# Performance work log

Measured on AMD Instinct MI355X. Metric: run time of the kernel, lower is better.

## Reference

```python
import jax, jax.numpy as jnp
import numpy as np

LN_EPS = 1e-5
ATT_EPS = 1e-6

def layer_norm(x, scale, bias):
    mu = jnp.mean(x, axis=-1, keepdims=True)
    var = jnp.mean(jnp.square(x - mu), axis=-1, keepdims=True)
    return (x - mu) * jax.lax.rsqrt(var + LN_EPS) * scale + bias

def setup_inputs() -> dict:
    key = jax.random.key(0)
    ks = jax.random.split(key, 8)
    N, C, H = 16384, 1024, 8
    s = 0.02
    return {
        "x": jax.random.normal(ks[0], (N, C), dtype=jnp.float32),
        "Wq": jax.random.normal(ks[1], (C, C), dtype=jnp.float32) * s,
        "Wkv": jax.random.normal(ks[2], (C, 2 * C), dtype=jnp.float32) * s,
        "ln1_scale": jnp.ones((C,), dtype=jnp.float32),
        "ln1_bias": jnp.zeros((C,), dtype=jnp.float32),
        "W1": jax.random.normal(ks[3], (C, C), dtype=jnp.float32) * s,
        "b1": jnp.zeros((C,), dtype=jnp.float32),
        "W2": jax.random.normal(ks[4], (C, C), dtype=jnp.float32) * s,
        "b2": jnp.zeros((C,), dtype=jnp.float32),
        "ln2_scale": jnp.ones((C,), dtype=jnp.float32),
        "ln2_bias": jnp.zeros((C,), dtype=jnp.float32),
    }

def reference(x, Wq, Wkv, ln1_scale, ln1_bias, W1, b1, W2, b2, ln2_scale, ln2_bias):
    H = 8
    N, C = x.shape
    d = C // H
    # QKV projections; torch .view(-1, d, heads) splits last dim as (d, H)
    q = (x @ Wq).reshape(N, d, H)
    kv = x @ Wkv  # [N, 2C]
    k = kv[:, :C].reshape(N, d, H)
    v = kv[:, C:].reshape(N, d, H)
    # Kernelized linear attention per head (phi = elu + 1), global segment (bi=None)
    phi_q = jax.nn.elu(q) + 1.0
    phi_k = jax.nn.elu(k) + 1.0
    kv_sum = jnp.einsum('ndh,neh->deh', phi_k, v)      # [d, d, H]
    z = jnp.sum(phi_k, axis=0)                          # [d, H]
    num = jnp.einsum('ndh,deh->neh', phi_q, kv_sum)     # [N, d, H]
    den = jnp.einsum('ndh,dh->nh', phi_q, z)            # [N, H]
    t = (num / (den[:, None, :] + ATT_EPS)).reshape(N, C)
    # AddNorm (beta=False, dropout=0): ln(t + x)
    y = layer_norm(t + x, ln1_scale, ln1_bias)
    # FFN: Linear -> GELU (exact) -> Linear
    h = jax.nn.gelu(y @ W1 + b1, approximate=False)
    f = h @ W2 + b2
    return layer_norm(f + y, ln2_scale, ln2_bias)
```

## Files before the change

kernel.cpp:

```cpp
#include <hip/hip_runtime.h>
#include <hip/hip_bf16.h>
#include <cstdint>
#include <cstddef>

typedef __bf16 bf16_t;
typedef bf16_t bf16x4 __attribute__((ext_vector_type(4)));
typedef bf16_t bf16x8 __attribute__((ext_vector_type(8)));
typedef float f32x4 __attribute__((ext_vector_type(4)));

static constexpr int NROWS = 16384;
static constexpr int CDIM  = 1024;

__device__ __forceinline__ int p6(int k) {
  return (k & 32) | ((k & 12) << 1) | ((k & 16) >> 2) | (k & 3);
}
__device__ __forceinline__ int p6i(int s) {
  return (s & 32) | ((s & 4) << 2) | ((s & 24) >> 1) | (s & 3);
}
__device__ __forceinline__ int permc(int c) {
  return (c & ~63) | p6(c & 63);
}


__device__ __forceinline__ void gload16(const bf16_t* g, bf16_t* l) {
  __builtin_amdgcn_global_load_lds((const __attribute__((address_space(1))) void*)g,
                                   (__attribute__((address_space(3))) void*)l, 16, 0, 0);
}

__device__ __forceinline__ bf16x8 ldsf128(const bf16_t* lds, int row, int ldbytes, int kbyte) {
  const char* p = (const char*)lds + row * ldbytes + (kbyte ^ ((row & 7) << 4));
  return *(const bf16x8*)p;
}

__device__ __forceinline__ float phi_fn(float v) {
  return v > 0.f ? v + 1.f : expf(v);
}
__device__ __forceinline__ float gelu_fn(float v) {
  return 0.5f * v * (1.f + erff(v * 0.70710678118654752f));
}


__global__ void cast_x_kernel(const float* __restrict__ x, bf16_t* __restrict__ xb, long nchunks) {
  long i = (long)blockIdx.x * blockDim.x + threadIdx.x;
  long stride = (long)gridDim.x * blockDim.x;
  for (long c = i; c < nchunks; c += stride) {
    long row = c >> 7;
    int p0 = (int)(c & 127) << 3;
    int group = p0 & ~63;
    int ccl = (p0 >> 3) & 7;
    int klo = ((ccl & 4) << 3) | ((ccl & 3) << 2);
    const float* src = x + row * 1024 + group + klo;
    float4 a = *(const float4*)src;
    float4 b = *(const float4*)(src + 16);
    bf16x8 o;
    o[0] = (bf16_t)a.x; o[1] = (bf16_t)a.y; o[2] = (bf16_t)a.z; o[3] = (bf16_t)a.w;
    o[4] = (bf16_t)b.x; o[5] = (bf16_t)b.y; o[6] = (bf16_t)b.z; o[7] = (bf16_t)b.w;
    *(bf16x8*)(xb + row * 1024 + p0) = o;
  }
}

__global__ void prep_w_kernel(const float* __restrict__ Wq, const float* __restrict__ Wkv,
                              const float* __restrict__ W1, const float* __restrict__ W2,
                              bf16_t* __restrict__ wqkv_bt, bf16_t* __restrict__ w1bt,
                              bf16_t* __restrict__ w2bt) {
  __shared__ float tile[64][65];
  int mode = blockIdx.z;
  const float* src; int ld; bf16_t* dst; int permute;
  if (mode == 0)      { src = Wq;          ld = 1024; dst = wqkv_bt;                       permute = 1; }
  else if (mode == 1) { src = Wkv;         ld = 2048; dst = wqkv_bt + (size_t)1024 * 1024; permute = 1; }
  else if (mode == 2) { src = Wkv + 1024;  ld = 2048; dst = wqkv_bt + (size_t)2048 * 1024; permute = 1; }
  else if (mode == 3) { src = W1;          ld = 1024; dst = w1bt;                          permute = 0; }
  else                { src = W2;          ld = 1024; dst = w2bt;                          permute = 0; }
  int r0 = blockIdx.x * 64, c0 = blockIdx.y * 64;
  int tid = threadIdx.x;
#pragma unroll
  for (int i = 0; i < 16; i++) {
    int idx = i * 256 + tid; int rr = idx >> 6, cc = idx & 63;
    tile[rr][cc] = src[(size_t)(r0 + rr) * ld + c0 + cc];
  }
  __syncthreads();
#pragma unroll
  for (int i = 0; i < 16; i++) {
    int idx = i * 256 + tid; int cc = idx >> 6, rr = idx & 63;
    int c = c0 + cc;
    int a = permute ? (((c & 7) << 7) | (c >> 3)) : c;
    dst[(size_t)a * 1024 + r0 + p6(rr)] = (bf16_t)tile[rr][cc];
  }
}


template<int MODE>
__global__ __launch_bounds__(256, 4)
void gemm_bt_kernel(const bf16_t* __restrict__ A, const bf16_t* __restrict__ Bt,
                    const float* __restrict__ bias,
                    bf16_t* __restrict__ o0, bf16_t* __restrict__ o1, bf16_t* __restrict__ o2,
                    int M, int N, int K)
{
  __shared__ bf16_t As[128 * 64];
  __shared__ bf16_t Bs[128 * 64];
  const int tid  = threadIdx.x;
  const int lane = tid & 63;
  const int wave = tid >> 6;
  const int wr = (wave >> 1) * 64, wc = (wave & 1) * 64;
  const int l15 = lane & 15, g = lane >> 4;
  const int row0 = blockIdx.x * 128, col0 = blockIdx.y * 128;
  const int cb = wave * 256;
  f32x4 acc[4][4] = {};

  for (int kt = 0; kt < K; kt += 64) {
    __syncthreads();
#pragma unroll
    for (int it = 0; it < 4; ++it) {
      int ch = cb + it * 64 + lane;
      int r = ch >> 3;
      int csrc = (ch & 7) ^ (r & 7);
      gload16(A  + (size_t)(row0 + r) * K + kt + csrc * 8, As + (size_t)(cb + it * 64) * 8);
      gload16(Bt + (size_t)(col0 + r) * K + kt + csrc * 8, Bs + (size_t)(cb + it * 64) * 8);
    }
    __syncthreads();
#pragma unroll
    for (int ks = 0; ks < 2; ++ks) {
      bf16x8 af[4], bfr[4];
#pragma unroll
      for (int i = 0; i < 4; i++) af[i]  = ldsf128(As, wr + i * 16 + l15, 128, ks * 64 + 16 * g);
#pragma unroll
      for (int i = 0; i < 4; i++) bfr[i] = ldsf128(Bs, wc + i * 16 + l15, 128, ks * 64 + 16 * g);
#pragma unroll
      for (int i = 0; i < 4; i++)
#pragma unroll
        for (int j = 0; j < 4; j++)
          acc[i][j] = __builtin_amdgcn_mfma_f32_16x16x32_bf16(af[i], bfr[j], acc[i][j], 0, 0, 0);
    }
  }

#pragma unroll
  for (int i = 0; i < 4; i++) {
    int rbase = row0 + wr + i * 16 + g * 4;
#pragma unroll
    for (int j = 0; j < 4; j++) {
      int col = col0 + wc + j * 16 + l15;
      f32x4 v = acc[i][j];
      if constexpr (MODE == 0) {
        int seg = col >> 10;
        int f   = col & 1023;
        if (seg == 0) {
          int cl = permc(f);
#pragma unroll
          for (int rr = 0; rr < 4; rr++)
            o0[(size_t)(rbase + rr) * 1024 + cl] = (bf16_t)phi_fn(v[rr]);
        } else {
          int tp = (rbase & ~63) | p6(rbase & 63);
          bf16x4 pack;
#pragma unroll
          for (int rr = 0; rr < 4; rr++)
            pack[rr] = (bf16_t)(seg == 1 ? phi_fn(v[rr]) : v[rr]);
          bf16_t* dst = (seg == 1) ? o1 : o2;
          *(bf16x4*)(dst + (size_t)f * 16384 + tp) = pack;
        }
      } else if constexpr (MODE == 1) {
        float bv = bias[col];
        int cs = permc(col);
#pragma unroll
        for (int rr = 0; rr < 4; rr++)
          o0[(size_t)(rbase + rr) * 1024 + cs] = (bf16_t)gelu_fn(v[rr] + bv);
      } else {
        float bv = bias[col];
#pragma unroll
        for (int rr = 0; rr < 4; rr++)
          o0[(size_t)(rbase + rr) * 1024 + col] = (bf16_t)(v[rr] + bv);
      }
    }
  }
}


__global__ __launch_bounds__(256, 4)
void kvsum_mfma_kernel(const bf16_t* __restrict__ phikT, const bf16_t* __restrict__ vT,
                       float* __restrict__ P)
{
  __shared__ bf16_t As[128 * 64];
  __shared__ bf16_t Bs[128 * 64];
  const int h = blockIdx.y, c = blockIdx.x;
  const bf16_t* A = phikT + (size_t)h * 128 * 16384;
  const bf16_t* B = vT    + (size_t)h * 128 * 16384;
  const int tid = threadIdx.x, lane = tid & 63, wave = tid >> 6;
  const int wr = (wave >> 1) * 64, wc = (wave & 1) * 64;
  const int l15 = lane & 15, g = lane >> 4;
  const int cb = wave * 256;
  f32x4 acc[4][4] = {};

  for (int kk = 0; kk < 4; ++kk) {
    const int kt = c * 256 + kk * 64;
    __syncthreads();
#pragma unroll
    for (int it = 0; it < 4; ++it) {
      int ch = cb + it * 64 + lane;
      int r = ch >> 3;
      int csrc = (ch & 7) ^ (r & 7);
      gload16(A + (size_t)r * 16384 + kt + csrc * 8, As + (size_t)(cb + it * 64) * 8);
      gload16(B + (size_t)r * 16384 + kt + csrc * 8, Bs + (size_t)(cb + it * 64) * 8);
    }
    __syncthreads();
#pragma unroll
    for (int ks = 0; ks < 2; ++ks) {
      bf16x8 af[4], bfr[4];
#pragma unroll
      for (int i = 0; i < 4; i++) af[i]  = ldsf128(As, wr + i * 16 + l15, 128, ks * 64 + 16 * g);
#pragma unroll
      for (int i = 0; i < 4; i++) bfr[i] = ldsf128(Bs, wc + i * 16 + l15, 128, ks * 64 + 16 * g);
#pragma unroll
      for (int i = 0; i < 4; i++)
#pragma unroll
        for (int j = 0; j < 4; j++)
          acc[i][j] = __builtin_amdgcn_mfma_f32_16x16x32_bf16(af[i], bfr[j], acc[i][j], 0, 0, 0);
    }
  }

  float* pb = P + ((size_t)h * 64 + c) * 16384;
#pragma unroll
  for (int i = 0; i < 4; i++) {
    int e = wr + i * 16 + g * 4;
#pragma unroll
    for (int j = 0; j < 4; j++) {
      int f = wc + j * 16 + l15;
      f32x4 v = acc[i][j];
#pragma unroll
      for (int rr = 0; rr < 4; rr++)
        pb[(size_t)(e + rr) * 128 + f] = v[rr];
    }
  }
}

__global__ void zsumT_kernel(const bf16_t* __restrict__ phikT, float* __restrict__ z) {
  __shared__ float red[4];
  int f = blockIdx.x, tid = threadIdx.x;
  const bf16_t* p = phikT + (size_t)f * 16384 + tid * 64;
  float s = 0.f;
#pragma unroll
  for (int j = 0; j < 8; j++) {
    bf16x8 v8 = *(const bf16x8*)(p + j * 8);
#pragma unroll
    for (int i = 0; i < 8; i++) s += (float)v8[i];
  }
#pragma unroll
  for (int o = 32; o > 0; o >>= 1) s += __shfl_down(s, o);
  if ((tid & 63) == 0) red[tid >> 6] = s;
  __syncthreads();
  if (tid == 0) z[f] = red[0] + red[1] + red[2] + red[3];
}

__global__ void reduce_kvsum_kernel(const float* __restrict__ P, bf16_t* __restrict__ Mbt)
{
  int i = blockIdx.x * 256 + threadIdx.x;
  int h = i >> 14, d = (i >> 7) & 127, f = i & 127;
  const float* p = P + (size_t)h * 64 * 16384 + (size_t)d * 128 + f;
  float s = 0.f;
#pragma unroll 8
  for (int c = 0; c < 64; ++c) s += p[(size_t)c * 16384];
  int ds = (d & 64) | p6(d & 63);
  Mbt[(size_t)h * 16384 + f * 128 + ds] = (bf16_t)s;
}


__global__ __launch_bounds__(256, 3)
void attn_t_kernel(const bf16_t* __restrict__ phiq, const bf16_t* __restrict__ Mbt,
                   const float* __restrict__ z, bf16_t* __restrict__ tout)
{
  __shared__ bf16_t As[64 * 128];
  __shared__ bf16_t Bs[128 * 128];
  __shared__ float  zs[128];
  __shared__ float  dens[64];
  int h = blockIdx.y, row0 = blockIdx.x * 64;
  int tid = threadIdx.x, lane = tid & 63, wave = tid >> 6;
  int wr = (wave >> 1) * 32, wc = (wave & 1) * 64;
  int l15 = lane & 15, g = lane >> 4;

#pragma unroll
  for (int it = 0; it < 4; ++it) {
    int ch = it * 256 + tid;
    int r = ch >> 4, c8 = ch & 15;
    int cs = c8 ^ (r & 7);
    *(bf16x8*)(As + r * 128 + cs * 8) = *(const bf16x8*)(phiq + (size_t)(row0 + r) * 1024 + h * 128 + c8 * 8);
  }
#pragma unroll
  for (int it = 0; it < 8; ++it) {
    int ch = it * 256 + tid;
    int r = ch >> 4, c8 = ch & 15;
    int cs = c8 ^ (r & 7);
    *(bf16x8*)(Bs + r * 128 + cs * 8) = *(const bf16x8*)(Mbt + (size_t)h * 16384 + ch * 8);
  }
  if (tid < 128) zs[tid] = z[h * 128 + ((tid & 64) | p6i(tid & 63))];
  __syncthreads();

  f32x4 acc[2][4] = {};
#pragma unroll
  for (int ks = 0; ks < 4; ++ks) {
    bf16x8 af[2], bfr[4];
#pragma unroll
    for (int i = 0; i < 2; i++) af[i]  = ldsf128(As, wr + i * 16 + l15, 256, ks * 64 + 16 * g);
#pragma unroll
    for (int j = 0; j < 4; j++) bfr[j] = ldsf128(Bs, wc + j * 16 + l15, 256, ks * 64 + 16 * g);
#pragma unroll
    for (int i = 0; i < 2; i++)
#pragma unroll
      for (int j = 0; j < 4; j++)
        acc[i][j] = __builtin_amdgcn_mfma_f32_16x16x32_bf16(af[i], bfr[j], acc[i][j], 0, 0, 0);
  }

  if (tid < 64) {
    float s = 0.f;
    const char* p = (const char*)As + tid * 256;
    int sw = (tid & 7) << 4;
    for (int d0 = 0; d0 < 128; ++d0) {
      int d = (d0 + tid) & 127;
      bf16_t kv = *(const bf16_t*)(p + ((2 * d) ^ sw));
      s += (float)kv * zs[d];
    }
    dens[tid] = s;
  }
  __syncthreads();

#pragma unroll
  for (int i = 0; i < 2; i++) {
    int lr = wr + i * 16 + g * 4;
#pragma unroll
    for (int j = 0; j < 4; j++) {
      int col = h * 128 + wc + j * 16 + l15;
      f32x4 v = acc[i][j];
#pragma unroll
      for (int rr = 0; rr < 4; rr++) {
        float den = dens[lr + rr] + 1e-6f;
        tout[(size_t)(row0 + lr + rr) * 1024 + col] = (bf16_t)(v[rr] / den);
      }
    }
  }
}


__global__ __launch_bounds__(256, 2)
void ln1_kernel(const bf16_t* __restrict__ t, const float* __restrict__ x,
                const float* __restrict__ gma, const float* __restrict__ bta,
                bf16_t* __restrict__ y)
{
  __shared__ float s[1024];
  __shared__ float rsum[4], rsq[4];
  int n = blockIdx.x, tid = threadIdx.x;
#pragma unroll
  for (int k = 0; k < 4; k++) {
    int p = k * 256 + tid;
    float tv = (float)t[(size_t)n * 1024 + p];
    int c = ((p & 127) << 3) | (p >> 7);
    s[c] = tv;
  }
  __syncthreads();
  float sum = 0.f, sq = 0.f, sv[4];
#pragma unroll
  for (int k = 0; k < 4; k++) {
    int c = k * 256 + tid;
    float v = s[c] + x[(size_t)n * 1024 + c];
    sv[k] = v; sum += v; sq += v * v;
  }
#pragma unroll
  for (int o = 32; o > 0; o >>= 1) { sum += __shfl_down(sum, o); sq += __shfl_down(sq, o); }
  if ((tid & 63) == 0) { rsum[tid >> 6] = sum; rsq[tid >> 6] = sq; }
  __syncthreads();
  sum = rsum[0] + rsum[1] + rsum[2] + rsum[3];
  sq  = rsq[0] + rsq[1] + rsq[2] + rsq[3];
  float mu = sum * (1.f / 1024.f);
  float var = sq * (1.f / 1024.f) - mu * mu;
  float rs = rsqrtf(var + 1e-5f);
#pragma unroll
  for (int k = 0; k < 4; k++) {
    int c = k * 256 + tid;
    y[(size_t)n * 1024 + permc(c)] = (bf16_t)((sv[k] - mu) * rs * gma[c] + bta[c]);
  }
}

__global__ __launch_bounds__(256, 2)
void ln2_kernel(const bf16_t* __restrict__ f, const bf16_t* __restrict__ y,
                const float* __restrict__ gma, const float* __restrict__ bta,
                float* __restrict__ out)
{
  __shared__ float rsum[4], rsq[4];
  int n = blockIdx.x, tid = threadIdx.x;
  float sum = 0.f, sq = 0.f, sv[4];
#pragma unroll
  for (int k = 0; k < 4; k++) {
    int c = k * 256 + tid;
    float v = (float)f[(size_t)n * 1024 + c] + (float)y[(size_t)n * 1024 + permc(c)];
    sv[k] = v; sum += v; sq += v * v;
  }
#pragma unroll
  for (int o = 32; o > 0; o >>= 1) { sum += __shfl_down(sum, o); sq += __shfl_down(sq, o); }
  if ((tid & 63) == 0) { rsum[tid >> 6] = sum; rsq[tid >> 6] = sq; }
  __syncthreads();
  sum = rsum[0] + rsum[1] + rsum[2] + rsum[3];
  sq  = rsq[0] + rsq[1] + rsq[2] + rsq[3];
  float mu = sum * (1.f / 1024.f);
  float var = sq * (1.f / 1024.f) - mu * mu;
  float rs = rsqrtf(var + 1e-5f);
#pragma unroll
  for (int k = 0; k < 4; k++) {
    int c = k * 256 + tid;
    out[(size_t)n * 1024 + c] = (sv[k] - mu) * rs * gma[c] + bta[c];
  }
}


extern "C" void kernel_launch(void* const* d_in, const int* in_sizes, int n_in,
                              void* d_out, int out_size, void* d_ws, size_t ws_size,
                              hipStream_t stream)
{
  const float* x    = (const float*)d_in[0];
  const float* Wq   = (const float*)d_in[1];
  const float* Wkv  = (const float*)d_in[2];
  const float* g1   = (const float*)d_in[3];
  const float* bt1  = (const float*)d_in[4];
  const float* W1   = (const float*)d_in[5];
  const float* b1   = (const float*)d_in[6];
  const float* W2   = (const float*)d_in[7];
  const float* b2   = (const float*)d_in[8];
  const float* g2   = (const float*)d_in[9];
  const float* bt2  = (const float*)d_in[10];
  float* out = (float*)d_out;

  char* ws = (char*)d_ws;
  size_t off = 0;
  auto alloc = [&](size_t bytes) { void* p = ws + off; off += (bytes + 255) & ~(size_t)255; return p; };

  const size_t NC2 = (size_t)NROWS * CDIM * 2;
  bf16_t* xb    = (bf16_t*)alloc(NC2);
  bf16_t* wqkv  = (bf16_t*)alloc((size_t)3072 * 1024 * 2);
  bf16_t* w1bt  = (bf16_t*)alloc((size_t)1024 * 1024 * 2);
  bf16_t* w2bt  = (bf16_t*)alloc((size_t)1024 * 1024 * 2);
  bf16_t* phiq  = (bf16_t*)alloc(NC2);
  bf16_t* phikT = (bf16_t*)alloc(NC2);
  bf16_t* vT    = (bf16_t*)alloc(NC2);
  bf16_t* ybuf  = (bf16_t*)alloc(NC2);
  float*  zbuf  = (float*)alloc(4096);
  bf16_t* Mbt   = (bf16_t*)alloc(262144);
  float*  Pbuf  = (float*)xb;
  bf16_t* tbuf  = xb;
  bf16_t* hbuf  = phikT;
  bf16_t* fbuf  = vT;

  cast_x_kernel<<<2048, 256, 0, stream>>>(x, xb, (long)NROWS * CDIM / 8);
  prep_w_kernel<<<dim3(16, 16, 5), 256, 0, stream>>>(Wq, Wkv, W1, W2, wqkv, w1bt, w2bt);

  gemm_bt_kernel<0><<<dim3(128, 24), 256, 0, stream>>>(xb, wqkv, nullptr, phiq, phikT, vT,
                                                       NROWS, 3072, 1024);
  kvsum_mfma_kernel<<<dim3(64, 8), 256, 0, stream>>>(phikT, vT, Pbuf);
  zsumT_kernel<<<1024, 256, 0, stream>>>(phikT, zbuf);
  reduce_kvsum_kernel<<<512, 256, 0, stream>>>(Pbuf, Mbt);
  attn_t_kernel<<<dim3(256, 8), 256, 0, stream>>>(phiq, Mbt, zbuf, tbuf);
  ln1_kernel<<<NROWS, 256, 0, stream>>>(tbuf, x, g1, bt1, ybuf);

  gemm_bt_kernel<1><<<dim3(128, 8), 256, 0, stream>>>(ybuf, w1bt, b1, hbuf, nullptr, nullptr,
                                                      NROWS, 1024, 1024);
  gemm_bt_kernel<2><<<dim3(128, 8), 256, 0, stream>>>(hbuf, w2bt, b2, fbuf, nullptr, nullptr,
                                                      NROWS, 1024, 1024);
  ln2_kernel<<<NROWS, 256, 0, stream>>>(fbuf, ybuf, g2, bt2, out);
}
```

Baseline: 325.6 us.

## Replace GEMM with 256x256-tile, 8-wave, 4-stage pipelined kernel

Replaces the 128x128 single-buffered GEMM with a 512-thread kernel that computes 256x256 output tiles, using a 4-slot LDS ring with loads prefetched two k-steps ahead. A and B stages are interleaved with the two half-tile MFMA phases, MFMA issue priority is raised with setprio, and block IDs are swizzled across 8 groups for cache locality. The intent is to hide global-load latency and double data reuse per block. In exchange it needs 128KB of LDS and one block per CU, relies on hardcoded K=1024 and manual vmcnt waits, and the LDS layout no longer uses the earlier XOR swizzle, which risks bank conflicts.

```diff
diff --git a/kernel.cpp b/kernel.cpp
--- a/kernel.cpp
+++ b/kernel.cpp
@@ -90,55 +90,101 @@
 
 
 template<int MODE>
-__global__ __launch_bounds__(256, 4)
-void gemm_bt_kernel(const bf16_t* __restrict__ A, const bf16_t* __restrict__ Bt,
-                    const float* __restrict__ bias,
-                    bf16_t* __restrict__ o0, bf16_t* __restrict__ o1, bf16_t* __restrict__ o2,
-                    int M, int N, int K)
-{
-  __shared__ bf16_t As[128 * 64];
-  __shared__ bf16_t Bs[128 * 64];
-  const int tid  = threadIdx.x;
-  const int lane = tid & 63;
-  const int wave = tid >> 6;
-  const int wr = (wave >> 1) * 64, wc = (wave & 1) * 64;
+__global__ __launch_bounds__(512, 1)
+void gemm8p_kernel(const bf16_t* __restrict__ A, const bf16_t* __restrict__ Bt,
+                   const float* __restrict__ bias,
+                   bf16_t* __restrict__ o0, bf16_t* __restrict__ o1, bf16_t* __restrict__ o2,
+                   int tn_count)
+{
+  __shared__ bf16_t lds[4 * 16384];
+  const int tid = threadIdx.x, lane = tid & 63, wave = tid >> 6;
   const int l15 = lane & 15, g = lane >> 4;
-  const int row0 = blockIdx.x * 128, col0 = blockIdx.y * 128;
-  const int cb = wave * 256;
-  f32x4 acc[4][4] = {};
-
-  for (int kt = 0; kt < K; kt += 64) {
-    __syncthreads();
-#pragma unroll
-    for (int it = 0; it < 4; ++it) {
-      int ch = cb + it * 64 + lane;
-      int r = ch >> 3;
-      int csrc = (ch & 7) ^ (r & 7);
-      gload16(A  + (size_t)(row0 + r) * K + kt + csrc * 8, As + (size_t)(cb + it * 64) * 8);
-      gload16(Bt + (size_t)(col0 + r) * K + kt + csrc * 8, Bs + (size_t)(cb + it * 64) * 8);
-    }
-    __syncthreads();
-#pragma unroll
-    for (int ks = 0; ks < 2; ++ks) {
+  const int cpx = gridDim.x >> 3;
+  int swz = (blockIdx.x & 7) * cpx + (blockIdx.x >> 3);
+  const int row0 = (swz / tn_count) * 256, col0 = (swz % tn_count) * 256;
+  const int wrb = (wave >> 2) * 8, wcb = (wave & 3) * 4;
+  f32x4 acc[8][4] = {};
+
+  const size_t aoff0 = (size_t)(row0 + wave * 16 + l15) * 1024 + g * 8;
+  const size_t aoff1 = aoff0 + (size_t)128 * 1024;
+  const size_t boff0 = (size_t)(col0 + wave * 16 + l15) * 1024 + g * 8;
+  const size_t boff1 = boff0 + (size_t)128 * 1024;
+  const int wd0 = wave * 512, wd1 = (wave + 8) * 512;
+
+  auto stageA = [&](int t) {
+    bf16_t* s = lds + (t & 3) * 16384;
+    gload16(A + aoff0 + t * 32, s + wd0);
+    gload16(A + aoff1 + t * 32, s + wd1);
+  };
+  auto stageB = [&](int t) {
+    bf16_t* s = lds + (t & 3) * 16384 + 8192;
+    gload16(Bt + boff0 + t * 32, s + wd0);
+    gload16(Bt + boff1 + t * 32, s + wd1);
+  };
+
+  stageA(0); stageB(0); stageA(1); stageB(1);
+  asm volatile("s_waitcnt vmcnt(4)" ::: "memory");
+  __builtin_amdgcn_sched_barrier(0);
+  __builtin_amdgcn_s_barrier();
+  __builtin_amdgcn_sched_barrier(0);
+
+  for (int t = 0; t < 32; ++t) {
+    const bf16_t* sA = lds + (t & 3) * 16384;
+    const bf16_t* sB = sA + 8192;
+
+    if (t < 30) stageA(t + 2);
+    {
       bf16x8 af[4], bfr[4];
 #pragma unroll
-      for (int i = 0; i < 4; i++) af[i]  = ldsf128(As, wr + i * 16 + l15, 128, ks * 64 + 16 * g);
-#pragma unroll
-      for (int i = 0; i < 4; i++) bfr[i] = ldsf128(Bs, wc + i * 16 + l15, 128, ks * 64 + 16 * g);
+      for (int i = 0; i < 4; i++) af[i]  = *(const bf16x8*)(sA + (wrb + i) * 512 + lane * 8);
+#pragma unroll
+      for (int j = 0; j < 4; j++) bfr[j] = *(const bf16x8*)(sB + (wcb + j) * 512 + lane * 8);
+      __builtin_amdgcn_sched_barrier(0);
+      __builtin_amdgcn_s_barrier();
+      __builtin_amdgcn_sched_barrier(0);
+      __builtin_amdgcn_s_setprio(1);
 #pragma unroll
       for (int i = 0; i < 4; i++)
 #pragma unroll
         for (int j = 0; j < 4; j++)
           acc[i][j] = __builtin_amdgcn_mfma_f32_16x16x32_bf16(af[i], bfr[j], acc[i][j], 0, 0, 0);
-    }
-  }
-
-#pragma unroll
-  for (int i = 0; i < 4; i++) {
-    int rbase = row0 + wr + i * 16 + g * 4;
+      __builtin_amdgcn_s_setprio(0);
+    }
+    __builtin_amdgcn_sched_barrier(0);
+    __builtin_amdgcn_s_barrier();
+    __builtin_amdgcn_sched_barrier(0);
+
+    if (t < 30) stageB(t + 2);
+    {
+      bf16x8 af[4], bfr[4];
+#pragma unroll
+      for (int i = 0; i < 4; i++) af[i]  = *(const bf16x8*)(sA + (wrb + 4 + i) * 512 + lane * 8);
+#pragma unroll
+      for (int j = 0; j < 4; j++) bfr[j] = *(const bf16x8*)(sB + (wcb + j) * 512 + lane * 8);
+      __builtin_amdgcn_sched_barrier(0);
+      __builtin_amdgcn_s_barrier();
+      __builtin_amdgcn_sched_barrier(0);
+      __builtin_amdgcn_s_setprio(1);
+#pragma unroll
+      for (int i = 0; i < 4; i++)
+#pragma unroll
+        for (int j = 0; j < 4; j++)
+          acc[4 + i][j] = __builtin_amdgcn_mfma_f32_16x16x32_bf16(af[i], bfr[j], acc[4 + i][j], 0, 0, 0);
+      __builtin_amdgcn_s_setprio(0);
+    }
+    if (t < 30)       asm volatile("s_waitcnt vmcnt(4)" ::: "memory");
+    else if (t == 30) asm volatile("s_waitcnt vmcnt(0)" ::: "memory");
+    __builtin_amdgcn_sched_barrier(0);
+    __builtin_amdgcn_s_barrier();
+    __builtin_amdgcn_sched_barrier(0);
+  }
+
+#pragma unroll
+  for (int i = 0; i < 8; i++) {
+    int rbase = row0 + (wave >> 2) * 128 + i * 16 + g * 4;
 #pragma unroll
     for (int j = 0; j < 4; j++) {
-      int col = col0 + wc + j * 16 + l15;
+      int col = col0 + (wave & 3) * 64 + j * 16 + l15;
       f32x4 v = acc[i][j];
       if constexpr (MODE == 0) {
         int seg = col >> 10;
@@ -447,17 +493,14 @@
   cast_x_kernel<<<2048, 256, 0, stream>>>(x, xb, (long)NROWS * CDIM / 8);
   prep_w_kernel<<<dim3(16, 16, 5), 256, 0, stream>>>(Wq, Wkv, W1, W2, wqkv, w1bt, w2bt);
 
-  gemm_bt_kernel<0><<<dim3(128, 24), 256, 0, stream>>>(xb, wqkv, nullptr, phiq, phikT, vT,
-                                                       NROWS, 3072, 1024);
+  gemm8p_kernel<0><<<64 * 12, 512, 0, stream>>>(xb, wqkv, nullptr, phiq, phikT, vT, 12);
   kvsum_mfma_kernel<<<dim3(64, 8), 256, 0, stream>>>(phikT, vT, Pbuf);
   zsumT_kernel<<<1024, 256, 0, stream>>>(phikT, zbuf);
   reduce_kvsum_kernel<<<512, 256, 0, stream>>>(Pbuf, Mbt);
   attn_t_kernel<<<dim3(256, 8), 256, 0, stream>>>(phiq, Mbt, zbuf, tbuf);
   ln1_kernel<<<NROWS, 256, 0, stream>>>(tbuf, x, g1, bt1, ybuf);
 
-  gemm_bt_kernel<1><<<dim3(128, 8), 256, 0, stream>>>(ybuf, w1bt, b1, hbuf, nullptr, nullptr,
-                                                      NROWS, 1024, 1024);
-  gemm_bt_kernel<2><<<dim3(128, 8), 256, 0, stream>>>(hbuf, w2bt, b2, fbuf, nullptr, nullptr,
-                                                      NROWS, 1024, 1024);
+  gemm8p_kernel<1><<<64 * 4, 512, 0, stream>>>(ybuf, w1bt, b1, hbuf, nullptr, nullptr, 4);
+  gemm8p_kernel<2><<<64 * 4, 512, 0, stream>>>(hbuf, w2bt, b2, fbuf, nullptr, nullptr, 4);
   ln2_kernel<<<NROWS, 256, 0, stream>>>(fbuf, ybuf, g2, bt2, out);
 }
```

Result: slower. 371.6 us (+14.1%).
